# Kernel tuning notes

Hardware: AMD Instinct MI355X
Metric: run time of the kernel (lower is better)

## Reference

```python
import jax, jax.numpy as jnp
import numpy as np

B, T, D, H = 4096, 48, 64, 128
IMPUTE_WEIGHT = 0.3


def setup_inputs() -> dict:
    key = jax.random.key(0)
    ks = jax.random.split(key, 16)
    values = jax.random.normal(ks[0], (B, T, D), dtype=jnp.float32)
    masks = (jax.random.uniform(ks[1], (B, T, D)) < 0.7).astype(jnp.float32)
    deltas = jax.random.uniform(ks[2], (B, T, D), dtype=jnp.float32)
    s = 0.05
    return {
        "values": values, "masks": masks, "deltas": deltas,
        # TemporalDecay h (non-diag): Linear(D -> H)
        "W_td_h": jax.random.normal(ks[3], (H, D), dtype=jnp.float32) * s,
        "b_td_h": jax.random.normal(ks[4], (H,), dtype=jnp.float32) * s,
        # TemporalDecay x (diag): W is D x D but only diagonal used
        "W_td_x": jax.random.normal(ks[5], (D, D), dtype=jnp.float32) * s,
        "b_td_x": jax.random.normal(ks[6], (D,), dtype=jnp.float32) * s,
        # hist_reg: Linear(H -> D)
        "W_hist": jax.random.normal(ks[7], (D, H), dtype=jnp.float32) * s,
        "b_hist": jax.random.normal(ks[8], (D,), dtype=jnp.float32) * s,
        # feat_reg: D x D with zeroed diagonal mask
        "W_feat": jax.random.normal(ks[9], (D, D), dtype=jnp.float32) * s,
        "b_feat": jax.random.normal(ks[10], (D,), dtype=jnp.float32) * s,
        # weight_combine: Linear(2D -> D)
        "W_comb": jax.random.normal(ks[11], (D, 2 * D), dtype=jnp.float32) * s,
        "b_comb": jax.random.normal(ks[12], (D,), dtype=jnp.float32) * s,
        # LSTMCell(2D -> H), torch gate order i,f,g,o
        "W_ih": jax.random.normal(ks[13], (4 * H, 2 * D), dtype=jnp.float32) * s,
        "W_hh": jax.random.normal(ks[14], (4 * H, H), dtype=jnp.float32) * s,
        "b_ih": jnp.zeros((4 * H,), dtype=jnp.float32),
        "b_hh": jnp.zeros((4 * H,), dtype=jnp.float32),
    }


def reference(values, masks, deltas, W_td_h, b_td_h, W_td_x, b_td_x,
              W_hist, b_hist, W_feat, b_feat, W_comb, b_comb,
              W_ih, W_hh, b_ih, b_hh):
    Bn, Tn, Dn = values.shape
    Hn = W_hh.shape[1]
    w_td_x_diag = jnp.diagonal(W_td_x)                      # diag mask -> elementwise
    W_feat_m = W_feat * (1.0 - jnp.eye(Dn, dtype=W_feat.dtype))  # zero diagonal

    def step(carry, xs):
        h, c, x_loss = carry
        x, m, d = xs                                        # each [B, D]
        gamma_h = jnp.exp(-jax.nn.relu(d @ W_td_h.T + b_td_h))   # [B, H]
        gamma_x = jnp.exp(-jax.nn.relu(d * w_td_x_diag + b_td_x))  # [B, D]
        h = h * gamma_h
        x_h = h @ W_hist.T + b_hist
        denom = jnp.sum(m) + 1e-5
        x_loss = x_loss + jnp.sum(jnp.abs(x - x_h) * m) / denom
        x_c = m * x + (1.0 - m) * x_h
        z_h = x_c @ W_feat_m.T + b_feat
        x_loss = x_loss + jnp.sum(jnp.abs(x - z_h) * m) / denom
        alpha = jnp.concatenate([gamma_x, m], axis=1) @ W_comb.T + b_comb
        c_h = alpha * z_h + (1.0 - alpha) * x_h
        x_loss = x_loss + jnp.sum(jnp.abs(x - c_h) * m) / denom
        c_c = m * x + (1.0 - m) * c_h
        inp = jnp.concatenate([c_c, m], axis=1)             # [B, 2D]
        gates = inp @ W_ih.T + b_ih + h @ W_hh.T + b_hh     # [B, 4H]
        i_g, f_g, g_g, o_g = jnp.split(gates, 4, axis=1)
        c = jax.nn.sigmoid(f_g) * c + jax.nn.sigmoid(i_g) * jnp.tanh(g_g)
        h = jax.nn.sigmoid(o_g) * jnp.tanh(c)
        return (h, c, x_loss), c_c

    h0 = jnp.zeros((Bn, Hn), dtype=values.dtype)
    c0 = jnp.zeros((Bn, Hn), dtype=values.dtype)
    xs = (jnp.swapaxes(values, 0, 1), jnp.swapaxes(masks, 0, 1), jnp.swapaxes(deltas, 0, 1))
    (_, _, x_loss), imps = jax.lax.scan(step, (h0, c0, jnp.float32(0.0)), xs)
    imputations = jnp.swapaxes(imps, 0, 1)                  # [B, T, D]
    loss = x_loss * IMPUTE_WEIGHT
    return loss, imputations
```

## Files before the change

kernel.cpp:

```cpp
#include <hip/hip_runtime.h>
#include <hip/hip_bf16.h>
#include <cmath>

#define Bb 4096
#define Tt 48
#define Dd 64
#define Hh 128
#define NB 16
#define NTHR 512

#define BAR_LDS() asm volatile("s_waitcnt lgkmcnt(0)\n\ts_barrier" ::: "memory")

typedef unsigned short ushort_t;
typedef __attribute__((ext_vector_type(8))) short short8;
typedef __attribute__((ext_vector_type(4))) float floatx4;

#define WS_DEN   0
#define WS_LOSS  48
#define WS_CNT   49
#define WS_FRAGS 64
#define FR_F 0
#define FR_A 256
#define FR_B 272
#define FR_C 288
#define FR_E 296
#define N_FRAGS 312
#define DENOM_BLOCKS (48 * 16)

__device__ __forceinline__ ushort_t f2bf(float x) {
  unsigned int u = __float_as_uint(x);
  u += 0x7fffu + ((u >> 16) & 1u);
  return (ushort_t)(u >> 16);
}
__device__ __forceinline__ unsigned int pack_bf2(float a, float b) {
  union { __hip_bfloat162 h; unsigned int u; } cv;
  cv.h = __float22bfloat162_rn(make_float2(a, b));
  return cv.u;
}
__device__ __forceinline__ float sigmoidf_(float x) { return 1.0f / (1.0f + __expf(-x)); }
__device__ __forceinline__ float tanhf_(float x) { return 2.0f / (1.0f + __expf(-2.0f * x)) - 1.0f; }

__global__ void prep_denom_kernel(const float* __restrict__ W_td_h, const float* __restrict__ W_hist,
                                  const float* __restrict__ W_feat, const float* __restrict__ W_comb,
                                  const float* __restrict__ W_ih, const float* __restrict__ W_hh,
                                  const float* __restrict__ masks, float* __restrict__ ws) {
  int tid = threadIdx.x;
  if (blockIdx.x < N_FRAGS) {
    int f = blockIdx.x;
    ushort_t* fb = (ushort_t*)(ws + WS_FRAGS);
    #pragma unroll
    for (int u = 0; u < 2; u++) {
      int e = tid * 2 + u;
      int l = e >> 3, j = e & 7;
      int n16 = l & 15;
      int kq = ((l >> 4) << 3) + j;
      float v;
      if (f < 256) {
        int w = f >> 5, g = (f >> 3) & 3, ks = f & 7;
        int n = g * 128 + w * 16 + n16;
        int k = ks * 32 + kq;
        v = (k < 128) ? W_ih[n * 128 + k] : W_hh[n * 128 + (k - 128)];
      } else if (f < 272) {
        int ff = f - 256, w = ff >> 1, ks = ff & 1;
        int n = w * 16 + n16;
        v = W_td_h[n * 64 + ks * 32 + kq];
      } else if (f < 288) {
        int ff = f - 272, w = ff >> 2, ks = ff & 3;
        int n = w * 16 + n16;
        v = W_hist[n * 128 + ks * 32 + kq];
      } else if (f < 296) {
        int ff = f - 288, w = ff >> 1, ks = ff & 1;
        int n = w * 16 + n16;
        int k = ks * 32 + kq;
        v = (n == k) ? 0.0f : W_feat[n * 64 + k];
      } else {
        int ff = f - 296, w = ff >> 2, ks = ff & 3;
        int n = w * 16 + n16;
        v = W_comb[n * 128 + ks * 32 + kq];
      }
      fb[f * 512 + e] = f2bf(v);
    }
  } else {
    int blk = blockIdx.x - N_FRAGS;
    int t = blk >> 4;
    int chunk = blk & 15;
    int base = chunk * 256;
    int j = tid & 63;
    int brow = tid >> 6;
    float s = 0.0f;
    for (int i = 0; i < 64; i++) {
      int b = base + i * 4 + brow;
      s += masks[((size_t)b * Tt + t) * Dd + j];
    }
    for (int off = 32; off > 0; off >>= 1) s += __shfl_down(s, off, 64);
    __shared__ float red[4];
    if ((tid & 63) == 0) red[tid >> 6] = s;
    __syncthreads();
    if (tid == 0) atomicAdd(&ws[WS_DEN + t], red[0] + red[1] + red[2] + red[3]);
  }
}

__global__ __launch_bounds__(NTHR, 2)
void main_kernel(const float* __restrict__ values, const float* __restrict__ masks,
                 const float* __restrict__ deltas, const float* __restrict__ W_td_x,
                 const float* __restrict__ b_td_h, const float* __restrict__ b_td_x,
                 const float* __restrict__ b_hist, const float* __restrict__ b_feat,
                 const float* __restrict__ b_comb,
                 const float* __restrict__ b_ih, const float* __restrict__ b_hh,
                 float* ws, float* __restrict__ out) {
  __shared__ __align__(16) ushort_t act[16 * 264];
  __shared__ __align__(16) ushort_t dbuf[16 * 72];
  __shared__ __align__(16) ushort_t gxbuf[16 * 72];
  __shared__ __align__(16) ushort_t xcbuf[16 * 72];
  __shared__ __align__(16) float xmbuf[16 * 132];
  __shared__ __align__(16) float xhbuf[16 * 68];
  __shared__ float sden[48];
  __shared__ float red[8];

  int tid = threadIdx.x;
  int w = tid >> 6;
  int lane = tid & 63;
  int l15 = lane & 15;
  int quad = lane >> 4;
  int b0 = blockIdx.x * NB;
  const ushort_t* fb = (const ushort_t*)(ws + WS_FRAGS);

  for (int i = tid; i < 48; i += NTHR) sden[i] = 1.0f / (ws[WS_DEN + i] + 1e-5f);

  short8 wF[32];
  #pragma unroll
  for (int g = 0; g < 4; g++)
    #pragma unroll
    for (int ks = 0; ks < 8; ks++)
      wF[g * 8 + ks] = *(const short8*)(fb + (size_t)(FR_F + w * 32 + g * 8 + ks) * 512 + lane * 8);
  short8 wA[2];
  #pragma unroll
  for (int ks = 0; ks < 2; ks++)
    wA[ks] = *(const short8*)(fb + (size_t)(FR_A + w * 2 + ks) * 512 + lane * 8);
  short8 wBE[4];
  short8 wC[2];
  if (w < 4) {
    #pragma unroll
    for (int ks = 0; ks < 4; ks++)
      wBE[ks] = *(const short8*)(fb + (size_t)(FR_B + w * 4 + ks) * 512 + lane * 8);
  } else {
    #pragma unroll
    for (int ks = 0; ks < 4; ks++)
      wBE[ks] = *(const short8*)(fb + (size_t)(FR_E + (w - 4) * 4 + ks) * 512 + lane * 8);
    #pragma unroll
    for (int ks = 0; ks < 2; ks++)
      wC[ks] = *(const short8*)(fb + (size_t)(FR_C + (w - 4) * 2 + ks) * 512 + lane * 8);
  }

  int colh = w * 16 + l15;
  float biasF0 = b_ih[colh]       + b_hh[colh];
  float biasF1 = b_ih[128 + colh] + b_hh[128 + colh];
  float biasF2 = b_ih[256 + colh] + b_hh[256 + colh];
  float biasF3 = b_ih[384 + colh] + b_hh[384 + colh];
  float biasA  = b_td_h[colh];
  int colD = (w & 3) * 16 + l15;
  float biasBE = (w < 4) ? b_hist[colD] : b_comb[colD];
  float biasC  = b_feat[colD];

  int e0 = tid * 2;
  int lb = e0 >> 6, li = e0 & 63;
  size_t gbase = ((size_t)(b0 + lb) * Tt) * Dd + li;
  float diag0 = W_td_x[li * 64 + li], diag1 = W_td_x[(li + 1) * 64 + (li + 1)];
  float btx0 = b_td_x[li], btx1 = b_td_x[li + 1];

  int ha[4];
  float* impp[4];
  #pragma unroll
  for (int r = 0; r < 4; r++) {
    int m = quad * 4 + r;
    ha[r] = m * 264 + 128 + colh;
    impp[r] = out + 1 + (size_t)(b0 + m) * Tt * Dd + colD;
  }

  float h_reg[4] = {0.f, 0.f, 0.f, 0.f};
  float c_reg[4] = {0.f, 0.f, 0.f, 0.f};
  float loss_acc = 0.0f;

  float2 px = *(const float2*)(values + gbase);
  float2 pm = *(const float2*)(masks + gbase);
  float2 pd = *(const float2*)(deltas + gbase);
  #pragma unroll
  for (int i = 0; i < 2; i++) {
    int e = tid + i * NTHR;
    *(unsigned int*)(&act[(e >> 6) * 264 + 128 + 2 * (e & 63)]) = 0u;
  }
  *(float4*)(&xmbuf[lb * 132 + 2 * li]) = make_float4(px.x, pm.x, px.y, pm.y);
  *(unsigned int*)(&act[lb * 264 + 64 + li]) = pack_bf2(pm.x, pm.y);
  {
    float g0 = __expf(-fmaxf(pd.x * diag0 + btx0, 0.0f));
    float g1 = __expf(-fmaxf(pd.y * diag1 + btx1, 0.0f));
    *(unsigned int*)(&gxbuf[lb * 72 + li]) = pack_bf2(g0, g1);
  }
  {
    size_t g = gbase + Dd;
    px = *(const float2*)(values + g);
    pm = *(const float2*)(masks + g);
    pd = *(const float2*)(deltas + g);
  }
  __syncthreads();

  for (int t = 0; t < Tt; t++) {
    float invden = sden[t];
    floatx4 a0 = {biasF0, biasF0, biasF0, biasF0};
    floatx4 a1 = {biasF1, biasF1, biasF1, biasF1};
    floatx4 a2 = {biasF2, biasF2, biasF2, biasF2};
    floatx4 a3 = {biasF3, biasF3, biasF3, biasF3};
    floatx4 accP = {biasBE, biasBE, biasBE, biasBE};

    short8 hf0 = *(const short8*)(&act[l15 * 264 + 128 + quad * 8]);
    short8 hf1 = *(const short8*)(&act[l15 * 264 + 160 + quad * 8]);
    short8 hf2 = *(const short8*)(&act[l15 * 264 + 192 + quad * 8]);
    short8 hf3 = *(const short8*)(&act[l15 * 264 + 224 + quad * 8]);
    short8 mf0 = *(const short8*)(&act[l15 * 264 + 64 + quad * 8]);
    short8 mf1 = *(const short8*)(&act[l15 * 264 + 96 + quad * 8]);
    if (w < 4) {
      accP = __builtin_amdgcn_mfma_f32_16x16x32_bf16(hf0, wBE[0], accP, 0, 0, 0);
      accP = __builtin_amdgcn_mfma_f32_16x16x32_bf16(hf1, wBE[1], accP, 0, 0, 0);
      accP = __builtin_amdgcn_mfma_f32_16x16x32_bf16(hf2, wBE[2], accP, 0, 0, 0);
      accP = __builtin_amdgcn_mfma_f32_16x16x32_bf16(hf3, wBE[3], accP, 0, 0, 0);
    } else {
      short8 gx0 = *(const short8*)(&gxbuf[l15 * 72 + quad * 8]);
      short8 gx1 = *(const short8*)(&gxbuf[l15 * 72 + 32 + quad * 8]);
      accP = __builtin_amdgcn_mfma_f32_16x16x32_bf16(gx0, wBE[0], accP, 0, 0, 0);
      accP = __builtin_amdgcn_mfma_f32_16x16x32_bf16(gx1, wBE[1], accP, 0, 0, 0);
      accP = __builtin_amdgcn_mfma_f32_16x16x32_bf16(mf0, wBE[2], accP, 0, 0, 0);
      accP = __builtin_amdgcn_mfma_f32_16x16x32_bf16(mf1, wBE[3], accP, 0, 0, 0);
    }
    a0 = __builtin_amdgcn_mfma_f32_16x16x32_bf16(mf0, wF[2],  a0, 0, 0, 0);
    a0 = __builtin_amdgcn_mfma_f32_16x16x32_bf16(mf1, wF[3],  a0, 0, 0, 0);
    a1 = __builtin_amdgcn_mfma_f32_16x16x32_bf16(mf0, wF[10], a1, 0, 0, 0);
    a1 = __builtin_amdgcn_mfma_f32_16x16x32_bf16(mf1, wF[11], a1, 0, 0, 0);
    a2 = __builtin_amdgcn_mfma_f32_16x16x32_bf16(mf0, wF[18], a2, 0, 0, 0);
    a2 = __builtin_amdgcn_mfma_f32_16x16x32_bf16(mf1, wF[19], a2, 0, 0, 0);
    a3 = __builtin_amdgcn_mfma_f32_16x16x32_bf16(mf0, wF[26], a3, 0, 0, 0);
    a3 = __builtin_amdgcn_mfma_f32_16x16x32_bf16(mf1, wF[27], a3, 0, 0, 0);
    a0 = __builtin_amdgcn_mfma_f32_16x16x32_bf16(hf0, wF[4],  a0, 0, 0, 0);
    a0 = __builtin_amdgcn_mfma_f32_16x16x32_bf16(hf1, wF[5],  a0, 0, 0, 0);
    a0 = __builtin_amdgcn_mfma_f32_16x16x32_bf16(hf2, wF[6],  a0, 0, 0, 0);
    a0 = __builtin_amdgcn_mfma_f32_16x16x32_bf16(hf3, wF[7],  a0, 0, 0, 0);
    a1 = __builtin_amdgcn_mfma_f32_16x16x32_bf16(hf0, wF[12], a1, 0, 0, 0);
    a1 = __builtin_amdgcn_mfma_f32_16x16x32_bf16(hf1, wF[13], a1, 0, 0, 0);
    a1 = __builtin_amdgcn_mfma_f32_16x16x32_bf16(hf2, wF[14], a1, 0, 0, 0);
    a1 = __builtin_amdgcn_mfma_f32_16x16x32_bf16(hf3, wF[15], a1, 0, 0, 0);
    a2 = __builtin_amdgcn_mfma_f32_16x16x32_bf16(hf0, wF[20], a2, 0, 0, 0);
    a2 = __builtin_amdgcn_mfma_f32_16x16x32_bf16(hf1, wF[21], a2, 0, 0, 0);
    a2 = __builtin_amdgcn_mfma_f32_16x16x32_bf16(hf2, wF[22], a2, 0, 0, 0);
    a2 = __builtin_amdgcn_mfma_f32_16x16x32_bf16(hf3, wF[23], a2, 0, 0, 0);
    a3 = __builtin_amdgcn_mfma_f32_16x16x32_bf16(hf0, wF[28], a3, 0, 0, 0);
    a3 = __builtin_amdgcn_mfma_f32_16x16x32_bf16(hf1, wF[29], a3, 0, 0, 0);
    a3 = __builtin_amdgcn_mfma_f32_16x16x32_bf16(hf2, wF[30], a3, 0, 0, 0);
    a3 = __builtin_amdgcn_mfma_f32_16x16x32_bf16(hf3, wF[31], a3, 0, 0, 0);
    if (w < 4) {
      float s1 = 0.0f;
      #pragma unroll
      for (int r = 0; r < 4; r++) {
        int m = quad * 4 + r;
        float2 xm = *(const float2*)(&xmbuf[m * 132 + 2 * colD]);
        float xh = accP[r];
        s1 += fabsf(xm.x - xh) * xm.y;
        xhbuf[m * 68 + colD] = xh;
        xcbuf[m * 72 + colD] = f2bf(xm.y * xm.x + (1.0f - xm.y) * xh);
      }
      loss_acc += s1 * invden;
    }
    BAR_LDS();

    if (w >= 4) {
      short8 xc0 = *(const short8*)(&xcbuf[l15 * 72 + quad * 8]);
      short8 xc1 = *(const short8*)(&xcbuf[l15 * 72 + 32 + quad * 8]);
      floatx4 accC = {biasC, biasC, biasC, biasC};
      accC = __builtin_amdgcn_mfma_f32_16x16x32_bf16(xc0, wC[0], accC, 0, 0, 0);
      accC = __builtin_amdgcn_mfma_f32_16x16x32_bf16(xc1, wC[1], accC, 0, 0, 0);
      float s23 = 0.0f;
      #pragma unroll
      for (int r = 0; r < 4; r++) {
        int m = quad * 4 + r;
        float2 xm = *(const float2*)(&xmbuf[m * 132 + 2 * colD]);
        float xh = xhbuf[m * 68 + colD];
        float zh = accC[r];
        float al = accP[r];
        s23 += fabsf(xm.x - zh) * xm.y;
        float ch = al * zh + (1.0f - al) * xh;
        s23 += fabsf(xm.x - ch) * xm.y;
        float cc = xm.y * xm.x + (1.0f - xm.y) * ch;
        *impp[r] = cc;
        impp[r] += Dd;
        act[m * 264 + colD] = f2bf(cc);
      }
      loss_acc += s23 * invden;
    }
    *(unsigned int*)(&dbuf[lb * 72 + li]) = pack_bf2(pd.x, pd.y);
    BAR_LDS();

    short8 cf0 = *(const short8*)(&act[l15 * 264 + quad * 8]);
    short8 cf1 = *(const short8*)(&act[l15 * 264 + 32 + quad * 8]);
    a0 = __builtin_amdgcn_mfma_f32_16x16x32_bf16(cf0, wF[0],  a0, 0, 0, 0);
    a0 = __builtin_amdgcn_mfma_f32_16x16x32_bf16(cf1, wF[1],  a0, 0, 0, 0);
    a1 = __builtin_amdgcn_mfma_f32_16x16x32_bf16(cf0, wF[8],  a1, 0, 0, 0);
    a1 = __builtin_amdgcn_mfma_f32_16x16x32_bf16(cf1, wF[9],  a1, 0, 0, 0);
    a2 = __builtin_amdgcn_mfma_f32_16x16x32_bf16(cf0, wF[16], a2, 0, 0, 0);
    a2 = __builtin_amdgcn_mfma_f32_16x16x32_bf16(cf1, wF[17], a2, 0, 0, 0);
    a3 = __builtin_amdgcn_mfma_f32_16x16x32_bf16(cf0, wF[24], a3, 0, 0, 0);
    a3 = __builtin_amdgcn_mfma_f32_16x16x32_bf16(cf1, wF[25], a3, 0, 0, 0);
    short8 df0 = *(const short8*)(&dbuf[l15 * 72 + quad * 8]);
    short8 df1 = *(const short8*)(&dbuf[l15 * 72 + 32 + quad * 8]);
    floatx4 accA = {biasA, biasA, biasA, biasA};
    accA = __builtin_amdgcn_mfma_f32_16x16x32_bf16(df0, wA[0], accA, 0, 0, 0);
    accA = __builtin_amdgcn_mfma_f32_16x16x32_bf16(df1, wA[1], accA, 0, 0, 0);
    #pragma unroll
    for (int r = 0; r < 4; r++) {
      float ig = sigmoidf_(a0[r]);
      float fg = sigmoidf_(a1[r]);
      float gg = tanhf_(a2[r]);
      float og = sigmoidf_(a3[r]);
      c_reg[r] = fg * c_reg[r] + ig * gg;
      h_reg[r] = og * tanhf_(c_reg[r]);
      float hd = h_reg[r] * __expf(-fmaxf(accA[r], 0.0f));
      act[ha[r]] = f2bf(hd);
    }
    *(float4*)(&xmbuf[lb * 132 + 2 * li]) = make_float4(px.x, pm.x, px.y, pm.y);
    *(unsigned int*)(&act[lb * 264 + 64 + li]) = pack_bf2(pm.x, pm.y);
    {
      float g0 = __expf(-fmaxf(pd.x * diag0 + btx0, 0.0f));
      float g1 = __expf(-fmaxf(pd.y * diag1 + btx1, 0.0f));
      *(unsigned int*)(&gxbuf[lb * 72 + li]) = pack_bf2(g0, g1);
    }
    {
      int tn = (t + 2 < Tt) ? (t + 2) : (Tt - 1);
      size_t g = gbase + (size_t)tn * Dd;
      px = *(const float2*)(values + g);
      pm = *(const float2*)(masks + g);
      pd = *(const float2*)(deltas + g);
    }
    BAR_LDS();
  }

  float s = loss_acc;
  for (int off = 32; off > 0; off >>= 1) s += __shfl_down(s, off, 64);
  if (lane == 0) red[w] = s;
  __syncthreads();
  if (tid == 0) {
    float tot = 0.0f;
    #pragma unroll
    for (int i = 0; i < 8; i++) tot += red[i];
    atomicAdd(&ws[WS_LOSS], tot);
    __threadfence();
    unsigned int done = atomicAdd((unsigned int*)&ws[WS_CNT], 1u);
    if (done == (unsigned int)(gridDim.x - 1)) {
      float lv = atomicAdd(&ws[WS_LOSS], 0.0f);
      out[0] = 0.3f * lv;
    }
  }
}

extern "C" void kernel_launch(void* const* d_in, const int* in_sizes, int n_in,
                              void* d_out, int out_size, void* d_ws, size_t ws_size,
                              hipStream_t stream) {
  const float* values = (const float*)d_in[0];
  const float* masks  = (const float*)d_in[1];
  const float* deltas = (const float*)d_in[2];
  const float* W_td_h = (const float*)d_in[3];
  const float* b_td_h = (const float*)d_in[4];
  const float* W_td_x = (const float*)d_in[5];
  const float* b_td_x = (const float*)d_in[6];
  const float* W_hist = (const float*)d_in[7];
  const float* b_hist = (const float*)d_in[8];
  const float* W_feat = (const float*)d_in[9];
  const float* b_feat = (const float*)d_in[10];
  const float* W_comb = (const float*)d_in[11];
  const float* b_comb = (const float*)d_in[12];
  const float* W_ih   = (const float*)d_in[13];
  const float* W_hh   = (const float*)d_in[14];
  const float* b_ih   = (const float*)d_in[15];
  const float* b_hh   = (const float*)d_in[16];
  float* out = (float*)d_out;
  float* ws  = (float*)d_ws;

  hipMemsetAsync(ws, 0, 64 * sizeof(float), stream);
  prep_denom_kernel<<<dim3(N_FRAGS + DENOM_BLOCKS), dim3(256), 0, stream>>>(
      W_td_h, W_hist, W_feat, W_comb, W_ih, W_hh, masks, ws);
  main_kernel<<<dim3(Bb / NB), dim3(NTHR), 0, stream>>>(values, masks, deltas, W_td_x,
                                                        b_td_h, b_td_x, b_hist, b_feat,
                                                        b_comb, b_ih, b_hh, ws, out);
}
```

Baseline: 397.6 us.

## Split LSTM gate work across 16 waves per block with LDS-staged weights

Doubles the block to 1024 threads so each wave computes two of the four LSTM gate groups instead of all four, halving per-wave MFMA chains and register-resident weight fragments. The hist/feat/comb projection weights are staged into dynamic shared memory instead of registers, and the auxiliary projections are handled by the upper eight waves. Gate pre-activations for g/o are exchanged through a new LDS buffer with an extra barrier per timestep. The intent is shorter per-step critical paths and lower register pressure, at the cost of more barriers, LDS traffic, and one block per CU.

```diff
diff --git a/kernel.cpp b/kernel.cpp
--- a/kernel.cpp
+++ b/kernel.cpp
@@ -7,13 +7,15 @@
 #define Dd 64
 #define Hh 128
 #define NB 16
-#define NTHR 512
+#define NTHR 1024
 
 #define BAR_LDS() asm volatile("s_waitcnt lgkmcnt(0)\n\ts_barrier" ::: "memory")
 
 typedef unsigned short ushort_t;
 typedef __attribute__((ext_vector_type(8))) short short8;
 typedef __attribute__((ext_vector_type(4))) float floatx4;
+
+#define MFMA __builtin_amdgcn_mfma_f32_16x16x32_bf16
 
 #define WS_DEN   0
 #define WS_LOSS  48
@@ -100,7 +102,7 @@
   }
 }
 
-__global__ __launch_bounds__(NTHR, 2)
+__global__ __launch_bounds__(NTHR, 1)
 void main_kernel(const float* __restrict__ values, const float* __restrict__ masks,
                  const float* __restrict__ deltas, const float* __restrict__ W_td_x,
                  const float* __restrict__ b_td_h, const float* __restrict__ b_td_x,
@@ -113,149 +115,132 @@
   __shared__ __align__(16) ushort_t gxbuf[16 * 72];
   __shared__ __align__(16) ushort_t xcbuf[16 * 72];
   __shared__ __align__(16) float xmbuf[16 * 132];
-  __shared__ __align__(16) float xhbuf[16 * 68];
+  __shared__ __align__(16) float gobuf[2 * 16 * 132];
+  __shared__ __align__(16) float albuf[16 * 68];
   __shared__ float sden[48];
-  __shared__ float red[8];
+  __shared__ float red[16];
+  extern __shared__ __align__(16) ushort_t wstage[];
 
   int tid = threadIdx.x;
   int w = tid >> 6;
   int lane = tid & 63;
   int l15 = lane & 15;
   int quad = lane >> 4;
+  int wcol = w & 7;
+  int gsel = w >> 3;
+  int gA = gsel * 2;
   int b0 = blockIdx.x * NB;
   const ushort_t* fb = (const ushort_t*)(ws + WS_FRAGS);
 
   for (int i = tid; i < 48; i += NTHR) sden[i] = 1.0f / (ws[WS_DEN + i] + 1e-5f);
-
-  short8 wF[32];
+  for (int i = tid; i < 40 * 512 / 8; i += NTHR)
+    *(short8*)(wstage + i * 8) = *(const short8*)(fb + (size_t)FR_B * 512 + i * 8);
+
+  short8 wF[16];
   #pragma unroll
-  for (int g = 0; g < 4; g++)
+  for (int g2 = 0; g2 < 2; g2++)
     #pragma unroll
     for (int ks = 0; ks < 8; ks++)
-      wF[g * 8 + ks] = *(const short8*)(fb + (size_t)(FR_F + w * 32 + g * 8 + ks) * 512 + lane * 8);
+      wF[g2 * 8 + ks] =
+          *(const short8*)(fb + (size_t)(FR_F + wcol * 32 + (gA + g2) * 8 + ks) * 512 + lane * 8);
   short8 wA[2];
-  #pragma unroll
-  for (int ks = 0; ks < 2; ks++)
-    wA[ks] = *(const short8*)(fb + (size_t)(FR_A + w * 2 + ks) * 512 + lane * 8);
-  short8 wBE[4];
-  short8 wC[2];
-  if (w < 4) {
-    #pragma unroll
-    for (int ks = 0; ks < 4; ks++)
-      wBE[ks] = *(const short8*)(fb + (size_t)(FR_B + w * 4 + ks) * 512 + lane * 8);
-  } else {
-    #pragma unroll
-    for (int ks = 0; ks < 4; ks++)
-      wBE[ks] = *(const short8*)(fb + (size_t)(FR_E + (w - 4) * 4 + ks) * 512 + lane * 8);
+  if (w < 8) {
     #pragma unroll
     for (int ks = 0; ks < 2; ks++)
-      wC[ks] = *(const short8*)(fb + (size_t)(FR_C + (w - 4) * 2 + ks) * 512 + lane * 8);
-  }
-
-  int colh = w * 16 + l15;
-  float biasF0 = b_ih[colh]       + b_hh[colh];
-  float biasF1 = b_ih[128 + colh] + b_hh[128 + colh];
-  float biasF2 = b_ih[256 + colh] + b_hh[256 + colh];
-  float biasF3 = b_ih[384 + colh] + b_hh[384 + colh];
-  float biasA  = b_td_h[colh];
-  int colD = (w & 3) * 16 + l15;
-  float biasBE = (w < 4) ? b_hist[colD] : b_comb[colD];
-  float biasC  = b_feat[colD];
-
-  int e0 = tid * 2;
-  int lb = e0 >> 6, li = e0 & 63;
-  size_t gbase = ((size_t)(b0 + lb) * Tt) * Dd + li;
-  float diag0 = W_td_x[li * 64 + li], diag1 = W_td_x[(li + 1) * 64 + (li + 1)];
-  float btx0 = b_td_x[li], btx1 = b_td_x[li + 1];
-
-  int ha[4];
-  float* impp[4];
-  #pragma unroll
-  for (int r = 0; r < 4; r++) {
-    int m = quad * 4 + r;
-    ha[r] = m * 264 + 128 + colh;
-    impp[r] = out + 1 + (size_t)(b0 + m) * Tt * Dd + colD;
-  }
-
-  float h_reg[4] = {0.f, 0.f, 0.f, 0.f};
+      wA[ks] = *(const short8*)(fb + (size_t)(FR_A + w * 2 + ks) * 512 + lane * 8);
+  }
+
+  int colh = wcol * 16 + l15;
+  float biasFa = b_ih[gA * 128 + colh] + b_hh[gA * 128 + colh];
+  float biasFb = b_ih[(gA + 1) * 128 + colh] + b_hh[(gA + 1) * 128 + colh];
+  float biasA = (w < 8) ? b_td_h[colh] : 0.0f;
+  int colD = (w >= 12) ? (wcol - 4) * 16 + l15 : wcol * 16 + l15;
+  float biasP = 0.0f, biasC = 0.0f;
+  if (w >= 12) biasP = b_comb[colD];
+  else if (w >= 8) { biasP = b_hist[colD]; biasC = b_feat[colD]; }
+
+  const ushort_t* wbe_p = wstage + (size_t)((w < 12) ? wcol * 4 : 24 + (wcol - 4) * 4) * 512 + lane * 8;
+  const ushort_t* wc_p  = wstage + (size_t)(16 + wcol * 2) * 512 + lane * 8;
+
+  int haB = quad * 4 * 264 + 128 + colh;
+  int off0 = 1 + (b0 + quad * 4) * Tt * Dd + colD;
+
   float c_reg[4] = {0.f, 0.f, 0.f, 0.f};
   float loss_acc = 0.0f;
 
-  float2 px = *(const float2*)(values + gbase);
-  float2 pm = *(const float2*)(masks + gbase);
-  float2 pd = *(const float2*)(deltas + gbase);
-  #pragma unroll
-  for (int i = 0; i < 2; i++) {
-    int e = tid + i * NTHR;
-    *(unsigned int*)(&act[(e >> 6) * 264 + 128 + 2 * (e & 63)]) = 0u;
-  }
-  *(float4*)(&xmbuf[lb * 132 + 2 * li]) = make_float4(px.x, pm.x, px.y, pm.y);
-  *(unsigned int*)(&act[lb * 264 + 64 + li]) = pack_bf2(pm.x, pm.y);
-  {
+  float2 px, pm, pd;
+  int lb = 0, li = 0;
+  size_t gbase = 0;
+  float diag0 = 0, diag1 = 0, btx0 = 0, btx1 = 0;
+  if (w >= 8) {
+    int e0 = (tid - 512) * 2;
+    lb = e0 >> 6; li = e0 & 63;
+    gbase = ((size_t)(b0 + lb) * Tt) * Dd + li;
+    diag0 = W_td_x[li * 64 + li]; diag1 = W_td_x[(li + 1) * 64 + (li + 1)];
+    btx0 = b_td_x[li]; btx1 = b_td_x[li + 1];
+    px = *(const float2*)(values + gbase);
+    pm = *(const float2*)(masks + gbase);
+    pd = *(const float2*)(deltas + gbase);
+    *(float4*)(&xmbuf[lb * 132 + 2 * li]) = make_float4(px.x, pm.x, px.y, pm.y);
+    *(unsigned int*)(&act[lb * 264 + 64 + li]) = pack_bf2(pm.x, pm.y);
     float g0 = __expf(-fmaxf(pd.x * diag0 + btx0, 0.0f));
     float g1 = __expf(-fmaxf(pd.y * diag1 + btx1, 0.0f));
     *(unsigned int*)(&gxbuf[lb * 72 + li]) = pack_bf2(g0, g1);
-  }
-  {
     size_t g = gbase + Dd;
     px = *(const float2*)(values + g);
     pm = *(const float2*)(masks + g);
     pd = *(const float2*)(deltas + g);
   }
+  {
+    int e = tid;
+    *(unsigned int*)(&act[(e >> 6) * 264 + 128 + 2 * (e & 63)]) = 0u;
+  }
   __syncthreads();
 
   for (int t = 0; t < Tt; t++) {
-    float invden = sden[t];
-    floatx4 a0 = {biasF0, biasF0, biasF0, biasF0};
-    floatx4 a1 = {biasF1, biasF1, biasF1, biasF1};
-    floatx4 a2 = {biasF2, biasF2, biasF2, biasF2};
-    floatx4 a3 = {biasF3, biasF3, biasF3, biasF3};
-    floatx4 accP = {biasBE, biasBE, biasBE, biasBE};
-
+    floatx4 aA = {biasFa, biasFa, biasFa, biasFa};
+    floatx4 aB = {biasFb, biasFb, biasFb, biasFb};
+    floatx4 accP = {biasP, biasP, biasP, biasP};
+
+    short8 mf0 = *(const short8*)(&act[l15 * 264 + 64 + quad * 8]);
+    short8 mf1 = *(const short8*)(&act[l15 * 264 + 96 + quad * 8]);
     short8 hf0 = *(const short8*)(&act[l15 * 264 + 128 + quad * 8]);
     short8 hf1 = *(const short8*)(&act[l15 * 264 + 160 + quad * 8]);
     short8 hf2 = *(const short8*)(&act[l15 * 264 + 192 + quad * 8]);
     short8 hf3 = *(const short8*)(&act[l15 * 264 + 224 + quad * 8]);
-    short8 mf0 = *(const short8*)(&act[l15 * 264 + 64 + quad * 8]);
-    short8 mf1 = *(const short8*)(&act[l15 * 264 + 96 + quad * 8]);
-    if (w < 4) {
-      accP = __builtin_amdgcn_mfma_f32_16x16x32_bf16(hf0, wBE[0], accP, 0, 0, 0);
-      accP = __builtin_amdgcn_mfma_f32_16x16x32_bf16(hf1, wBE[1], accP, 0, 0, 0);
-      accP = __builtin_amdgcn_mfma_f32_16x16x32_bf16(hf2, wBE[2], accP, 0, 0, 0);
-      accP = __builtin_amdgcn_mfma_f32_16x16x32_bf16(hf3, wBE[3], accP, 0, 0, 0);
-    } else {
-      short8 gx0 = *(const short8*)(&gxbuf[l15 * 72 + quad * 8]);
-      short8 gx1 = *(const short8*)(&gxbuf[l15 * 72 + 32 + quad * 8]);
-      accP = __builtin_amdgcn_mfma_f32_16x16x32_bf16(gx0, wBE[0], accP, 0, 0, 0);
-      accP = __builtin_amdgcn_mfma_f32_16x16x32_bf16(gx1, wBE[1], accP, 0, 0, 0);
-      accP = __builtin_amdgcn_mfma_f32_16x16x32_bf16(mf0, wBE[2], accP, 0, 0, 0);
-      accP = __builtin_amdgcn_mfma_f32_16x16x32_bf16(mf1, wBE[3], accP, 0, 0, 0);
-    }
-    a0 = __builtin_amdgcn_mfma_f32_16x16x32_bf16(mf0, wF[2],  a0, 0, 0, 0);
-    a0 = __builtin_amdgcn_mfma_f32_16x16x32_bf16(mf1, wF[3],  a0, 0, 0, 0);
-    a1 = __builtin_amdgcn_mfma_f32_16x16x32_bf16(mf0, wF[10], a1, 0, 0, 0);
-    a1 = __builtin_amdgcn_mfma_f32_16x16x32_bf16(mf1, wF[11], a1, 0, 0, 0);
-    a2 = __builtin_amdgcn_mfma_f32_16x16x32_bf16(mf0, wF[18], a2, 0, 0, 0);
-    a2 = __builtin_amdgcn_mfma_f32_16x16x32_bf16(mf1, wF[19], a2, 0, 0, 0);
-    a3 = __builtin_amdgcn_mfma_f32_16x16x32_bf16(mf0, wF[26], a3, 0, 0, 0);
-    a3 = __builtin_amdgcn_mfma_f32_16x16x32_bf16(mf1, wF[27], a3, 0, 0, 0);
-    a0 = __builtin_amdgcn_mfma_f32_16x16x32_bf16(hf0, wF[4],  a0, 0, 0, 0);
-    a0 = __builtin_amdgcn_mfma_f32_16x16x32_bf16(hf1, wF[5],  a0, 0, 0, 0);
-    a0 = __builtin_amdgcn_mfma_f32_16x16x32_bf16(hf2, wF[6],  a0, 0, 0, 0);
-    a0 = __builtin_amdgcn_mfma_f32_16x16x32_bf16(hf3, wF[7],  a0, 0, 0, 0);
-    a1 = __builtin_amdgcn_mfma_f32_16x16x32_bf16(hf0, wF[12], a1, 0, 0, 0);
-    a1 = __builtin_amdgcn_mfma_f32_16x16x32_bf16(hf1, wF[13], a1, 0, 0, 0);
-    a1 = __builtin_amdgcn_mfma_f32_16x16x32_bf16(hf2, wF[14], a1, 0, 0, 0);
-    a1 = __builtin_amdgcn_mfma_f32_16x16x32_bf16(hf3, wF[15], a1, 0, 0, 0);
-    a2 = __builtin_amdgcn_mfma_f32_16x16x32_bf16(hf0, wF[20], a2, 0, 0, 0);
-    a2 = __builtin_amdgcn_mfma_f32_16x16x32_bf16(hf1, wF[21], a2, 0, 0, 0);
-    a2 = __builtin_amdgcn_mfma_f32_16x16x32_bf16(hf2, wF[22], a2, 0, 0, 0);
-    a2 = __builtin_amdgcn_mfma_f32_16x16x32_bf16(hf3, wF[23], a2, 0, 0, 0);
-    a3 = __builtin_amdgcn_mfma_f32_16x16x32_bf16(hf0, wF[28], a3, 0, 0, 0);
-    a3 = __builtin_amdgcn_mfma_f32_16x16x32_bf16(hf1, wF[29], a3, 0, 0, 0);
-    a3 = __builtin_amdgcn_mfma_f32_16x16x32_bf16(hf2, wF[30], a3, 0, 0, 0);
-    a3 = __builtin_amdgcn_mfma_f32_16x16x32_bf16(hf3, wF[31], a3, 0, 0, 0);
-    if (w < 4) {
+    if (w >= 8) {
+      short8 wb0 = *(const short8*)(wbe_p);
+      short8 wb1 = *(const short8*)(wbe_p + 512);
+      short8 wb2 = *(const short8*)(wbe_p + 1024);
+      short8 wb3 = *(const short8*)(wbe_p + 1536);
+      if (w < 12) {
+        accP = MFMA(hf0, wb0, accP, 0, 0, 0);
+        accP = MFMA(hf1, wb1, accP, 0, 0, 0);
+        accP = MFMA(hf2, wb2, accP, 0, 0, 0);
+        accP = MFMA(hf3, wb3, accP, 0, 0, 0);
+      } else {
+        short8 gx0 = *(const short8*)(&gxbuf[l15 * 72 + quad * 8]);
+        short8 gx1 = *(const short8*)(&gxbuf[l15 * 72 + 32 + quad * 8]);
+        accP = MFMA(gx0, wb0, accP, 0, 0, 0);
+        accP = MFMA(gx1, wb1, accP, 0, 0, 0);
+        accP = MFMA(mf0, wb2, accP, 0, 0, 0);
+        accP = MFMA(mf1, wb3, accP, 0, 0, 0);
+      }
+    }
+    aA = MFMA(mf0, wF[2],  aA, 0, 0, 0);
+    aA = MFMA(mf1, wF[3],  aA, 0, 0, 0);
+    aB = MFMA(mf0, wF[10], aB, 0, 0, 0);
+    aB = MFMA(mf1, wF[11], aB, 0, 0, 0);
+    aA = MFMA(hf0, wF[4],  aA, 0, 0, 0);
+    aA = MFMA(hf1, wF[5],  aA, 0, 0, 0);
+    aA = MFMA(hf2, wF[6],  aA, 0, 0, 0);
+    aA = MFMA(hf3, wF[7],  aA, 0, 0, 0);
+    aB = MFMA(hf0, wF[12], aB, 0, 0, 0);
+    aB = MFMA(hf1, wF[13], aB, 0, 0, 0);
+    aB = MFMA(hf2, wF[14], aB, 0, 0, 0);
+    aB = MFMA(hf3, wF[15], aB, 0, 0, 0);
+    if (w >= 8 && w < 12) {
+      float invden = sden[t];
       float s1 = 0.0f;
       #pragma unroll
       for (int r = 0; r < 4; r++) {
@@ -263,79 +248,94 @@
         float2 xm = *(const float2*)(&xmbuf[m * 132 + 2 * colD]);
         float xh = accP[r];
         s1 += fabsf(xm.x - xh) * xm.y;
-        xhbuf[m * 68 + colD] = xh;
         xcbuf[m * 72 + colD] = f2bf(xm.y * xm.x + (1.0f - xm.y) * xh);
       }
       loss_acc += s1 * invden;
+    } else if (w >= 12) {
+      #pragma unroll
+      for (int r = 0; r < 4; r++)
+        albuf[(quad * 4 + r) * 68 + colD] = accP[r];
     }
     BAR_LDS();
 
-    if (w >= 4) {
+    if (w >= 8 && w < 12) {
       short8 xc0 = *(const short8*)(&xcbuf[l15 * 72 + quad * 8]);
       short8 xc1 = *(const short8*)(&xcbuf[l15 * 72 + 32 + quad * 8]);
+      short8 wc0 = *(const short8*)(wc_p);
+      short8 wc1 = *(const short8*)(wc_p + 512);
       floatx4 accC = {biasC, biasC, biasC, biasC};
-      accC = __builtin_amdgcn_mfma_f32_16x16x32_bf16(xc0, wC[0], accC, 0, 0, 0);
-      accC = __builtin_amdgcn_mfma_f32_16x16x32_bf16(xc1, wC[1], accC, 0, 0, 0);
+      accC = MFMA(xc0, wc0, accC, 0, 0, 0);
+      accC = MFMA(xc1, wc1, accC, 0, 0, 0);
+      float invden = sden[t];
       float s23 = 0.0f;
+      int tofs = t * 64;
       #pragma unroll
       for (int r = 0; r < 4; r++) {
         int m = quad * 4 + r;
         float2 xm = *(const float2*)(&xmbuf[m * 132 + 2 * colD]);
-        float xh = xhbuf[m * 68 + colD];
+        float xh = accP[r];
         float zh = accC[r];
-        float al = accP[r];
+        float al = albuf[m * 68 + colD];
         s23 += fabsf(xm.x - zh) * xm.y;
         float ch = al * zh + (1.0f - al) * xh;
         s23 += fabsf(xm.x - ch) * xm.y;
         float cc = xm.y * xm.x + (1.0f - xm.y) * ch;
-        *impp[r] = cc;
-        impp[r] += Dd;
+        out[off0 + r * 3072 + tofs] = cc;
         act[m * 264 + colD] = f2bf(cc);
       }
       loss_acc += s23 * invden;
     }
-    *(unsigned int*)(&dbuf[lb * 72 + li]) = pack_bf2(pd.x, pd.y);
+    if (w >= 8)
+      *(unsigned int*)(&dbuf[lb * 72 + li]) = pack_bf2(pd.x, pd.y);
     BAR_LDS();
 
     short8 cf0 = *(const short8*)(&act[l15 * 264 + quad * 8]);
     short8 cf1 = *(const short8*)(&act[l15 * 264 + 32 + quad * 8]);
-    a0 = __builtin_amdgcn_mfma_f32_16x16x32_bf16(cf0, wF[0],  a0, 0, 0, 0);
-    a0 = __builtin_amdgcn_mfma_f32_16x16x32_bf16(cf1, wF[1],  a0, 0, 0, 0);
-    a1 = __builtin_amdgcn_mfma_f32_16x16x32_bf16(cf0, wF[8],  a1, 0, 0, 0);
-    a1 = __builtin_amdgcn_mfma_f32_16x16x32_bf16(cf1, wF[9],  a1, 0, 0, 0);
-    a2 = __builtin_amdgcn_mfma_f32_16x16x32_bf16(cf0, wF[16], a2, 0, 0, 0);
-    a2 = __builtin_amdgcn_mfma_f32_16x16x32_bf16(cf1, wF[17], a2, 0, 0, 0);
-    a3 = __builtin_amdgcn_mfma_f32_16x16x32_bf16(cf0, wF[24], a3, 0, 0, 0);
-    a3 = __builtin_amdgcn_mfma_f32_16x16x32_bf16(cf1, wF[25], a3, 0, 0, 0);
-    short8 df0 = *(const short8*)(&dbuf[l15 * 72 + quad * 8]);
-    short8 df1 = *(const short8*)(&dbuf[l15 * 72 + 32 + quad * 8]);
+    aA = MFMA(cf0, wF[0],  aA, 0, 0, 0);
+    aA = MFMA(cf1, wF[1],  aA, 0, 0, 0);
+    aB = MFMA(cf0, wF[8],  aB, 0, 0, 0);
+    aB = MFMA(cf1, wF[9],  aB, 0, 0, 0);
     floatx4 accA = {biasA, biasA, biasA, biasA};
-    accA = __builtin_amdgcn_mfma_f32_16x16x32_bf16(df0, wA[0], accA, 0, 0, 0);
-    accA = __builtin_amdgcn_mfma_f32_16x16x32_bf16(df1, wA[1], accA, 0, 0, 0);
-    #pragma unroll
-    for (int r = 0; r < 4; r++) {
-      float ig = sigmoidf_(a0[r]);
-      float fg = sigmoidf_(a1[r]);
-      float gg = tanhf_(a2[r]);
-      float og = sigmoidf_(a3[r]);
-      c_reg[r] = fg * c_reg[r] + ig * gg;
-      h_reg[r] = og * tanhf_(c_reg[r]);
-      float hd = h_reg[r] * __expf(-fmaxf(accA[r], 0.0f));
-      act[ha[r]] = f2bf(hd);
-    }
-    *(float4*)(&xmbuf[lb * 132 + 2 * li]) = make_float4(px.x, pm.x, px.y, pm.y);
-    *(unsigned int*)(&act[lb * 264 + 64 + li]) = pack_bf2(pm.x, pm.y);
-    {
+    if (w < 8) {
+      short8 df0 = *(const short8*)(&dbuf[l15 * 72 + quad * 8]);
+      short8 df1 = *(const short8*)(&dbuf[l15 * 72 + 32 + quad * 8]);
+      accA = MFMA(df0, wA[0], accA, 0, 0, 0);
+      accA = MFMA(df1, wA[1], accA, 0, 0, 0);
+    } else {
+      #pragma unroll
+      for (int r = 0; r < 4; r++) {
+        int m = quad * 4 + r;
+        gobuf[m * 132 + colh] = aA[r];
+        gobuf[2112 + m * 132 + colh] = aB[r];
+      }
+      *(float4*)(&xmbuf[lb * 132 + 2 * li]) = make_float4(px.x, pm.x, px.y, pm.y);
+      *(unsigned int*)(&act[lb * 264 + 64 + li]) = pack_bf2(pm.x, pm.y);
       float g0 = __expf(-fmaxf(pd.x * diag0 + btx0, 0.0f));
       float g1 = __expf(-fmaxf(pd.y * diag1 + btx1, 0.0f));
       *(unsigned int*)(&gxbuf[lb * 72 + li]) = pack_bf2(g0, g1);
-    }
-    {
       int tn = (t + 2 < Tt) ? (t + 2) : (Tt - 1);
       size_t g = gbase + (size_t)tn * Dd;
       px = *(const float2*)(values + g);
       pm = *(const float2*)(masks + g);
       pd = *(const float2*)(deltas + g);
+    }
+    BAR_LDS();
+
+    if (w < 8) {
+      #pragma unroll
+      for (int r = 0; r < 4; r++) {
+        int m = quad * 4 + r;
+        float gg = gobuf[m * 132 + colh];
+        float og = gobuf[2112 + m * 132 + colh];
+        float ig = sigmoidf_(aA[r]);
+        float fg = sigmoidf_(aB[r]);
+        float g_ = tanhf_(gg);
+        float o_ = sigmoidf_(og);
+        c_reg[r] = fg * c_reg[r] + ig * g_;
+        float h_ = o_ * tanhf_(c_reg[r]);
+        float hd = h_ * __expf(-fmaxf(accA[r], 0.0f));
+        act[haB + r * 264] = f2bf(hd);
+      }
     }
     BAR_LDS();
   }
@@ -347,7 +347,7 @@
   if (tid == 0) {
     float tot = 0.0f;
     #pragma unroll
-    for (int i = 0; i < 8; i++) tot += red[i];
+    for (int i = 0; i < 16; i++) tot += red[i];
     atomicAdd(&ws[WS_LOSS], tot);
     __threadfence();
     unsigned int done = atomicAdd((unsigned int*)&ws[WS_CNT], 1u);
@@ -384,7 +384,7 @@
   hipMemsetAsync(ws, 0, 64 * sizeof(float), stream);
   prep_denom_kernel<<<dim3(N_FRAGS + DENOM_BLOCKS), dim3(256), 0, stream>>>(
       W_td_h, W_hist, W_feat, W_comb, W_ih, W_hh, masks, ws);
-  main_kernel<<<dim3(Bb / NB), dim3(NTHR), 0, stream>>>(values, masks, deltas, W_td_x,
-                                                        b_td_h, b_td_x, b_hist, b_feat,
-                                                        b_comb, b_ih, b_hh, ws, out);
-}
+  main_kernel<<<dim3(Bb / NB), dim3(NTHR), 40 * 512 * sizeof(ushort_t), stream>>>(
+      values, masks, deltas, W_td_x, b_td_h, b_td_x, b_hist, b_feat,
+      b_comb, b_ih, b_hh, ws, out);
+}
```

Measured after the change: 623.5 us. 56.8% more time.
